# Kernel optimization log

Hardware: AMD Instinct MI355X
Metric: run time of the kernel (lower is better)

The kernel has to match this reference:

```python
import jax, jax.numpy as jnp
import numpy as np

N_EMBD = 512
N_HEAD = 8
EPS = 1e-5


def setup_inputs() -> dict:
    key = jax.random.key(0)
    ks = jax.random.split(key, 8)
    C = N_EMBD
    s = lambda k, shape, fan: jax.random.normal(k, shape, jnp.float32) * (1.0 / np.sqrt(fan))
    return {
        "x": jax.random.normal(ks[0], (2, 4096, C), jnp.float32),
        "w_qkv": s(ks[1], (C, 3 * C), C), "b_qkv": jnp.zeros((3 * C,), jnp.float32),
        "w_attn_proj": s(ks[2], (C, C), C), "b_attn_proj": jnp.zeros((C,), jnp.float32),
        "w_fc": s(ks[3], (C, 4 * C), C), "b_fc": jnp.zeros((4 * C,), jnp.float32),
        "w_mlp_proj": s(ks[4], (4 * C, C), 4 * C), "b_mlp_proj": jnp.zeros((C,), jnp.float32),
        "ln1_g": jnp.ones((C,), jnp.float32), "ln1_b": jnp.zeros((C,), jnp.float32),
        "ln2_g": jnp.ones((C,), jnp.float32), "ln2_b": jnp.zeros((C,), jnp.float32),
    }


def _layernorm(x, g, b):
    mu = jnp.mean(x, axis=-1, keepdims=True)
    var = jnp.mean(jnp.square(x - mu), axis=-1, keepdims=True)
    return (x - mu) * jax.lax.rsqrt(var + EPS) * g + b


def _attention(x, w_qkv, b_qkv, w_proj, b_proj):
    B, T, C = x.shape
    hd = C // N_HEAD
    qkv = x @ w_qkv + b_qkv  # [B,T,3C]
    q, k, v = jnp.split(qkv, 3, axis=-1)
    q = q.reshape(B, T, N_HEAD, hd)
    k = k.reshape(B, T, N_HEAD, hd)
    v = v.reshape(B, T, N_HEAD, hd)
    # NOTE: faithful to source -- scale by sqrt(C) (n_embd), not sqrt(head_dim)
    scores = jnp.einsum('bthd,bshd->bhts', q, k) / jnp.sqrt(jnp.float32(C))
    mask = jnp.tril(jnp.ones((T, T), bool))
    scores = jnp.where(mask, scores, -jnp.inf)
    attn = jax.nn.softmax(scores, axis=-1)  # [B,H,T,T]
    y = jnp.einsum('bhts,bshd->bthd', attn, v).reshape(B, T, C)
    return y @ w_proj + b_proj


def _mlp(x, w_fc, b_fc, w_proj, b_proj):
    h = jax.nn.gelu(x @ w_fc + b_fc, approximate=True)
    return h @ w_proj + b_proj


def reference(x, w_qkv, b_qkv, w_attn_proj, b_attn_proj, w_fc, b_fc,
              w_mlp_proj, b_mlp_proj, ln1_g, ln1_b, ln2_g, ln2_b):
    x = x + _attention(_layernorm(x, ln1_g, ln1_b), w_qkv, b_qkv, w_attn_proj, b_attn_proj)
    x = x + _mlp(_layernorm(x, ln2_g, ln2_b), w_fc, b_fc, w_mlp_proj, b_mlp_proj)
    return x
```

## Files before the change

kernel.cpp:

```cpp
#include <hip/hip_runtime.h>
#include <hip/hip_bf16.h>
#include <math.h>

constexpr int B_ = 2;
constexpr int T_ = 4096;
constexpr int C_ = 512;
constexpr int H_ = 8;
constexpr int BT_ = B_ * T_;
constexpr float EPS_ = 1e-5f;

typedef __attribute__((ext_vector_type(8))) short bf16x8;
typedef __attribute__((ext_vector_type(4))) short short4v;
typedef __attribute__((ext_vector_type(8))) short short8v;
typedef __attribute__((ext_vector_type(4))) float f32x4;

__device__ __forceinline__ short f2bf(float f) {
    unsigned int u = __float_as_uint(f);
    unsigned int r = (u + 0x7fffu + ((u >> 16) & 1u)) >> 16;
    return (short)r;
}
__device__ __forceinline__ float bf2f(short s) {
    return __uint_as_float(((unsigned)(unsigned short)s) << 16);
}
__device__ __forceinline__ short f2bf_h(float f) {
    union { __hip_bfloat16 h; short s; } u;
    u.h = __float2bfloat16(f);
    return u.s;
}
__device__ __forceinline__ float exp2_f(float x) {
    float r;
    asm("v_exp_f32 %0, %1" : "=v"(r) : "v"(x));
    return r;
}

__device__ __forceinline__ float gelu_f(float v) {
    const float k0 = 0.7978845608028654f;
    const float k1 = 0.044715f;
    return 0.5f * v * (1.0f + tanhf(k0 * (v + k1 * v * v * v)));
}

__device__ __forceinline__ void gl_lds16(const short* gsrc, short* lds) {
    __builtin_amdgcn_global_load_lds(
        (const __attribute__((address_space(1))) void*)gsrc,
        (__attribute__((address_space(3))) void*)lds, 16, 0, 0);
}

__global__ __launch_bounds__(256) void transpose_w4(
    const float* __restrict__ W0, short* __restrict__ D0,
    const float* __restrict__ W1, short* __restrict__ D1,
    const float* __restrict__ W2, short* __restrict__ D2,
    const float* __restrict__ W3, short* __restrict__ D3) {
    __shared__ float tile[32][33];
    int bid = blockIdx.x;
    const float* W; short* D; int K, N, nx;
    if (bid < 768)       {             W = W0; D = D0; K = 512;  N = 1536; nx = 48; }
    else if (bid < 1024) { bid -= 768;  W = W1; D = D1; K = 512;  N = 512;  nx = 16; }
    else if (bid < 2048) { bid -= 1024; W = W2; D = D2; K = 512;  N = 2048; nx = 64; }
    else                 { bid -= 2048; W = W3; D = D3; K = 2048; N = 512;  nx = 16; }
    const int n0 = (bid % nx) * 32, k0 = (bid / nx) * 32;
    const int tx = threadIdx.x & 31, ty = threadIdx.x >> 5;
    #pragma unroll
    for (int j = 0; j < 4; j++)
        tile[ty + j * 8][tx] = W[(size_t)(k0 + ty + j * 8) * N + n0 + tx];
    __syncthreads();
    #pragma unroll
    for (int j = 0; j < 4; j++)
        D[(size_t)(n0 + ty + j * 8) * K + k0 + tx] = f2bf(tile[tx][ty + j * 8]);
}

__global__ __launch_bounds__(256) void ln_bf16(const float* __restrict__ x,
                                               const float* __restrict__ g,
                                               const float* __restrict__ b,
                                               short* __restrict__ out) {
    const int row = blockIdx.x * 4 + (threadIdx.x >> 6);
    const int lane = threadIdx.x & 63;
    const float* xr = x + (size_t)row * C_;

    float4 v0 = *(const float4*)(xr + lane * 8);
    float4 v1 = *(const float4*)(xr + lane * 8 + 4);

    float s  = v0.x + v0.y + v0.z + v0.w + v1.x + v1.y + v1.z + v1.w;
    float s2 = v0.x*v0.x + v0.y*v0.y + v0.z*v0.z + v0.w*v0.w
             + v1.x*v1.x + v1.y*v1.y + v1.z*v1.z + v1.w*v1.w;
    #pragma unroll
    for (int off = 32; off; off >>= 1) {
        s  += __shfl_down(s, off);
        s2 += __shfl_down(s2, off);
    }
    s  = __shfl(s, 0);
    s2 = __shfl(s2, 0);

    const float mu  = s * (1.0f / C_);
    const float var = s2 * (1.0f / C_) - mu * mu;
    const float rs  = rsqrtf(var + EPS_);

    float4 g0 = *(const float4*)(g + lane * 8);
    float4 g1 = *(const float4*)(g + lane * 8 + 4);
    float4 b0 = *(const float4*)(b + lane * 8);
    float4 b1 = *(const float4*)(b + lane * 8 + 4);

    short8v o;
    o[0] = f2bf((v0.x - mu) * rs * g0.x + b0.x);
    o[1] = f2bf((v0.y - mu) * rs * g0.y + b0.y);
    o[2] = f2bf((v0.z - mu) * rs * g0.z + b0.z);
    o[3] = f2bf((v0.w - mu) * rs * g0.w + b0.w);
    o[4] = f2bf((v1.x - mu) * rs * g1.x + b1.x);
    o[5] = f2bf((v1.y - mu) * rs * g1.y + b1.y);
    o[6] = f2bf((v1.z - mu) * rs * g1.z + b1.z);
    o[7] = f2bf((v1.w - mu) * rs * g1.w + b1.w);
    *(short8v*)(out + (size_t)row * C_ + lane * 8) = o;
}

template<int BM, int ACT, int OUTBF16, int HASRES, int VFUSE>
__global__ __launch_bounds__(256) void gemm_bf16(const short* __restrict__ A,
                                                 const short* __restrict__ Wt,
                                                 const float* __restrict__ bias,
                                                 const float* __restrict__ res,
                                                 void* __restrict__ outp,
                                                 int M, int N, int K,
                                                 int GX, int CY,
                                                 short* __restrict__ vtb) {
    constexpr int BK   = (BM == 128) ? 64 : 128;
    constexpr int MT   = BM / 32;
    constexpr int JMAX = BK / 32;
    constexpr int CPR  = BK / 8;
    constexpr int RPI  = 256 / CPR;
    constexpr int AISS = BM / RPI;
    constexpr int BISS = 128 / RPI;

    __shared__ short As[BM * BK];
    __shared__ short Bs[128 * BK];

    const int bid = blockIdx.x;
    const int xcd = bid & 7, jb = bid >> 3;
    const int by = xcd * CY + jb / GX;
    const int bx = jb % GX;

    const int t = threadIdx.x;
    const int w = t >> 6;
    const int l = t & 63;
    const int c = l & 15;
    const int g = l >> 4;
    const int wr = w >> 1, wc = w & 1;
    const int m0 = by * BM, n0 = bx * 128;

    const int rt  = t / CPR;
    const int sch = ((t % CPR) ^ (rt & 7)) * 8;
    const short* Asrc = A  + (size_t)(m0 + rt) * K + sch;
    const short* Bsrc = Wt + (size_t)(n0 + rt) * K + sch;

    auto stage = [&](int kt) {
        #pragma unroll
        for (int i = 0; i < AISS; i++)
            gl_lds16(Asrc + (size_t)(RPI * i) * K + kt, &As[i * 2048 + w * 512]);
        #pragma unroll
        for (int i = 0; i < BISS; i++)
            gl_lds16(Bsrc + (size_t)(RPI * i) * K + kt, &Bs[i * 2048 + w * 512]);
    };

    f32x4 acc[MT][4] = {};

    for (int kt = 0; kt < K; kt += BK) {
        stage(kt);
        __syncthreads();

        #pragma unroll
        for (int j = 0; j < JMAX; j++) {
            const int ckj = ((4 * j + g) ^ (c & 7)) * 8;
            bf16x8 af[MT], bfr[4];
            #pragma unroll
            for (int mt = 0; mt < MT; mt++)
                af[mt] = *(const bf16x8*)&As[(wr * (BM / 2) + mt * 16 + c) * BK + ckj];
            #pragma unroll
            for (int nt = 0; nt < 4; nt++)
                bfr[nt] = *(const bf16x8*)&Bs[(wc * 64 + nt * 16 + c) * BK + ckj];
            #pragma unroll
            for (int mt = 0; mt < MT; mt++)
                #pragma unroll
                for (int nt = 0; nt < 4; nt++)
                    acc[mt][nt] = __builtin_amdgcn_mfma_f32_16x16x32_bf16(
                        af[mt], bfr[nt], acc[mt][nt], 0, 0, 0);
        }

        __syncthreads();
    }

    const int colb = n0 + wc * 64;
    float bias_v[4];
    #pragma unroll
    for (int nt = 0; nt < 4; nt++) bias_v[nt] = bias[colb + nt * 16 + c];

    if (VFUSE && n0 >= 1024) {
        const int bq   = m0 >> 12;
        const int trow = (m0 & 4095) + wr * (BM / 2);
        #pragma unroll
        for (int mt = 0; mt < MT; mt++) {
            const int tb = trow + (mt >> 1) * 32 + 8 * g + 4 * (mt & 1);
            #pragma unroll
            for (int nt = 0; nt < 4; nt++) {
                const int vcol = colb + nt * 16 + c - 1024;
                const int hh = vcol >> 6, dd = vcol & 63;
                short4v pk;
                #pragma unroll
                for (int rr = 0; rr < 4; rr++)
                    pk[rr] = f2bf(acc[mt][nt][rr] + bias_v[nt]);
                *(short4v*)&vtb[((size_t)((bq * 8 + hh) * 64 + dd)) * T_ + tb] = pk;
            }
        }
        return;
    }

    float* out_f = (float*)outp;
    short* out_h = (short*)outp;

    #pragma unroll
    for (int mt = 0; mt < MT; mt++) {
        #pragma unroll
        for (int rr = 0; rr < 4; rr++) {
            const size_t row = (size_t)(m0 + wr * (BM / 2) + mt * 16 + 4 * g + rr);
            #pragma unroll
            for (int nt = 0; nt < 4; nt++) {
                const int col = colb + nt * 16 + c;
                float v = acc[mt][nt][rr] + bias_v[nt];
                if (ACT) v = gelu_f(v);
                if (HASRES) v += res[row * N + col];
                if (OUTBF16) out_h[row * N + col] = f2bf(v);
                else         out_f[row * N + col] = v;
            }
        }
    }
}

__global__ __launch_bounds__(256) void attn_mfma(const short* __restrict__ qkv,
                                                 const short* __restrict__ Vt,
                                                 short* __restrict__ y) {
    __shared__ union {
        struct { short K[2][64 * 64]; short V[2][64 * 64]; } s;
        float O[4][16][68];
    } sm;

    const int bid = blockIdx.x;
    const int xcd = bid & 7, jj = bid >> 3;
    const int lo = jj >> 6;
    const int qtr = jj & 63;
    const int qt = (qtr < 32) ? (63 - qtr) : (qtr - 32);
    const int g16 = xcd * 2 + lo;
    const int b = g16 >> 3, h = g16 & 7;

    const int tid = threadIdx.x, w = tid >> 6, lid = tid & 63;
    const int c = lid & 15, g = lid >> 4;
    const size_t base = (size_t)b * T_;
    const int bh = g16;

    const float qmul = 0.04419417382415922f * 1.4426950408889634f;

    bf16x8 qf0, qf1;
    {
        const short* qa = qkv + (base + qt * 64 + w * 16 + c) * 1536 + h * 64 + g * 8;
        bf16x8 a0 = *(const bf16x8*)qa;
        bf16x8 a1 = *(const bf16x8*)(qa + 32);
        #pragma unroll
        for (int i = 0; i < 8; i++) {
            qf0[i] = f2bf_h(bf2f(a0[i]) * qmul);
            qf1[i] = f2bf_h(bf2f(a1[i]) * qmul);
        }
    }

    const f32x4 kZero = {0.f, 0.f, 0.f, 0.f};
    bf16x8 kOnes;
    #pragma unroll
    for (int i = 0; i < 8; i++) kOnes[i] = (short)0x3F80;

    f32x4 ot[4] = {};
    f32x4 lacc = {0.f, 0.f, 0.f, 0.f};
    const int qg = qt * 64 + w * 16 + c;

    const int sr = tid >> 3;
    const int sc = ((tid & 7) ^ (sr & 7)) * 8;

    auto stage = [&](short* Kb, short* Vb, int st) {
        const short* ks = qkv + (base + st * 64 + sr) * 1536 + 512 + h * 64 + sc;
        const short* vs = Vt + ((size_t)(bh * 64 + sr)) * T_ + st * 64 + sc;
        gl_lds16(ks, Kb + w * 512);
        gl_lds16(ks + (size_t)32 * 1536, Kb + 2048 + w * 512);
        gl_lds16(vs, Vb + w * 512);
        gl_lds16(vs + (size_t)32 * T_, Vb + 2048 + w * 512);
    };

    const int rx = c & 7;
    const int ck0 = g ^ rx;
    const int ck1 = ck0 ^ 4;

    auto tile = [&](const short* Kb, const short* Vb, bool mask_diag) {
        f32x4 s[4];
        __builtin_amdgcn_s_setprio(1);
        #pragma unroll
        for (int mt = 0; mt < 4; mt++) {
            const short* krow = Kb + (mt * 16 + c) * 64;
            bf16x8 k0 = *(const bf16x8*)&krow[ck0 * 8];
            bf16x8 k1 = *(const bf16x8*)&krow[ck1 * 8];
            f32x4 z = __builtin_amdgcn_mfma_f32_16x16x32_bf16(k0, qf0, kZero, 0, 0, 0);
            s[mt] = __builtin_amdgcn_mfma_f32_16x16x32_bf16(k1, qf1, z, 0, 0, 0);
        }
        __builtin_amdgcn_s_setprio(0);

        float p[4][4];
        #pragma unroll
        for (int mt = 0; mt < 4; mt++)
            #pragma unroll
            for (int rr = 0; rr < 4; rr++) {
                float v = s[mt][rr];
                if (mask_diag && (qt * 64 + mt * 16 + 4 * g + rr > qg)) v = -1e30f;
                p[mt][rr] = exp2_f(v);
            }

        bf16x8 pb0, pb1;
        #pragma unroll
        for (int i = 0; i < 8; i++) {
            pb0[i] = f2bf_h(p[(i >> 2)][i & 3]);
            pb1[i] = f2bf_h(p[2 + (i >> 2)][i & 3]);
        }
        __builtin_amdgcn_s_setprio(1);
        lacc = __builtin_amdgcn_mfma_f32_16x16x32_bf16(kOnes, pb0, lacc, 0, 0, 0);
        lacc = __builtin_amdgcn_mfma_f32_16x16x32_bf16(kOnes, pb1, lacc, 0, 0, 0);
        #pragma unroll
        for (int dt = 0; dt < 4; dt++) {
            const short* vrow = Vb + (16 * dt + c) * 64;
            bf16x8 va0 = *(const bf16x8*)&vrow[ck0 * 8];
            bf16x8 va1 = *(const bf16x8*)&vrow[ck1 * 8];
            ot[dt] = __builtin_amdgcn_mfma_f32_16x16x32_bf16(va0, pb0, ot[dt], 0, 0, 0);
            ot[dt] = __builtin_amdgcn_mfma_f32_16x16x32_bf16(va1, pb1, ot[dt], 0, 0, 0);
        }
        __builtin_amdgcn_s_setprio(0);
    };

    short* K0 = sm.s.K[0]; short* K1 = sm.s.K[1];
    short* V0 = sm.s.V[0]; short* V1 = sm.s.V[1];

    stage(K0, V0, 0);
    asm volatile("s_waitcnt vmcnt(0)" ::: "memory");
    __syncthreads();

    int st = 0;
    while (st + 2 <= qt) {
        stage(K1, V1, st + 1);
        tile(K0, V0, false);
        asm volatile("s_waitcnt vmcnt(0)" ::: "memory");
        __syncthreads();
        stage(K0, V0, st + 2);
        tile(K1, V1, false);
        asm volatile("s_waitcnt vmcnt(0)" ::: "memory");
        __syncthreads();
        st += 2;
    }
    if (st < qt) {
        stage(K1, V1, st + 1);
        tile(K0, V0, false);
        asm volatile("s_waitcnt vmcnt(0)" ::: "memory");
        __syncthreads();
        tile(K1, V1, true);
    } else {
        tile(K0, V0, true);
    }
    __syncthreads();

    const float inv = 1.0f / lacc[0];
    #pragma unroll
    for (int dt = 0; dt < 4; dt++)
        #pragma unroll
        for (int rr = 0; rr < 4; rr++)
            sm.O[w][c][16 * dt + 4 * g + rr] = ot[dt][rr] * inv;
    const int q = lid >> 2, ch = lid & 3;
    short* dst = y + (base + qt * 64 + w * 16 + q) * 512 + h * 64 + ch * 16;
    short8v o0, o1;
    #pragma unroll
    for (int j = 0; j < 8; j++) o0[j] = f2bf(sm.O[w][q][ch * 16 + j]);
    #pragma unroll
    for (int j = 0; j < 8; j++) o1[j] = f2bf(sm.O[w][q][ch * 16 + 8 + j]);
    *(short8v*)dst = o0;
    *(short8v*)(dst + 8) = o1;
}

extern "C" void kernel_launch(void* const* d_in, const int* in_sizes, int n_in,
                              void* d_out, int out_size, void* d_ws, size_t ws_size,
                              hipStream_t stream) {
    const float* x           = (const float*)d_in[0];
    const float* w_qkv       = (const float*)d_in[1];
    const float* b_qkv       = (const float*)d_in[2];
    const float* w_attn_proj = (const float*)d_in[3];
    const float* b_attn_proj = (const float*)d_in[4];
    const float* w_fc        = (const float*)d_in[5];
    const float* b_fc        = (const float*)d_in[6];
    const float* w_mlp_proj  = (const float*)d_in[7];
    const float* b_mlp_proj  = (const float*)d_in[8];
    const float* ln1_g       = (const float*)d_in[9];
    const float* ln1_b       = (const float*)d_in[10];
    const float* ln2_g       = (const float*)d_in[11];
    const float* ln2_b       = (const float*)d_in[12];

    float* out = (float*)d_out;
    short* ws16 = (short*)d_ws;

    short* wqkvT = ws16;
    short* waT   = wqkvT + 1536 * 512;
    short* wfcT  = waT   + 512 * 512;
    short* wmT   = wfcT  + 2048 * 512;
    short* xn    = wmT   + 512 * 2048;
    short* ybuf  = xn    + (size_t)BT_ * 512;
    short* qkvh  = ybuf  + (size_t)BT_ * 512;
    short* vtb   = qkvh  + (size_t)BT_ * 2048;

    transpose_w4<<<3072, 256, 0, stream>>>(w_qkv, wqkvT, w_attn_proj, waT,
                                           w_fc, wfcT, w_mlp_proj, wmT);

    ln_bf16<<<BT_ / 4, 256, 0, stream>>>(x, ln1_g, ln1_b, xn);

    gemm_bf16<128, 0, 1, 0, 1><<<12 * 64, 256, 0, stream>>>(
        xn, wqkvT, b_qkv, nullptr, qkvh, BT_, 1536, 512, 12, 8, vtb);

    attn_mfma<<<1024, 256, 0, stream>>>(qkvh, vtb, ybuf);

    gemm_bf16<64, 0, 0, 1, 0><<<4 * 128, 256, 0, stream>>>(
        ybuf, waT, b_attn_proj, x, out, BT_, 512, 512, 4, 16, nullptr);

    ln_bf16<<<BT_ / 4, 256, 0, stream>>>(out, ln2_g, ln2_b, xn);

    gemm_bf16<128, 1, 1, 0, 0><<<16 * 64, 256, 0, stream>>>(
        xn, wfcT, b_fc, nullptr, qkvh, BT_, 2048, 512, 16, 8, nullptr);

    gemm_bf16<64, 0, 0, 1, 0><<<4 * 128, 256, 0, stream>>>(
        qkvh, wmT, b_mlp_proj, out, out, BT_, 512, 2048, 4, 16, nullptr);
}
```

Measured before the change: 175.2 us.

## Split-K the MLP down-projection with atomics and shrink GEMM row tiles

Adds a SPLITK template option to the bf16 GEMM. Each block handles half of K and atomically adds its partial sums into the fp32 output, which already holds the residual, and only the first half adds the bias. The MLP down-projection (K=2048) now launches twice as many blocks, and the QKV and FC GEMMs move from 128-row to 64-row tiles for more blocks. The goal is better CU occupancy and load balance, at the cost of many global fp32 atomics, more redundant B-tile loads, and a nondeterministic summation order.

```diff
diff --git a/kernel.cpp b/kernel.cpp
--- a/kernel.cpp
+++ b/kernel.cpp
@@ -111,7 +111,7 @@
     *(short8v*)(out + (size_t)row * C_ + lane * 8) = o;
 }
 
-template<int BM, int ACT, int OUTBF16, int HASRES, int VFUSE>
+template<int BM, int ACT, int OUTBF16, int HASRES, int VFUSE, int SPLITK>
 __global__ __launch_bounds__(256) void gemm_bf16(const short* __restrict__ A,
                                                  const short* __restrict__ Wt,
                                                  const float* __restrict__ bias,
@@ -132,7 +132,10 @@
     __shared__ short Bs[128 * BK];
 
     const int bid = blockIdx.x;
-    const int xcd = bid & 7, jb = bid >> 3;
+    const int xcd = bid & 7;
+    int jb = bid >> 3;
+    int koff = 0;
+    if (SPLITK) { koff = (jb & 1) * (K >> 1); jb >>= 1; }
     const int by = xcd * CY + jb / GX;
     const int bx = jb % GX;
 
@@ -160,7 +163,8 @@
 
     f32x4 acc[MT][4] = {};
 
-    for (int kt = 0; kt < K; kt += BK) {
+    const int kend = SPLITK ? (koff + (K >> 1)) : K;
+    for (int kt = koff; kt < kend; kt += BK) {
         stage(kt);
         __syncthreads();
 
@@ -212,6 +216,24 @@
 
     float* out_f = (float*)outp;
     short* out_h = (short*)outp;
+
+    if (SPLITK) {
+        const bool addb = (koff == 0);
+        #pragma unroll
+        for (int mt = 0; mt < MT; mt++) {
+            #pragma unroll
+            for (int rr = 0; rr < 4; rr++) {
+                const size_t row = (size_t)(m0 + wr * (BM / 2) + mt * 16 + 4 * g + rr);
+                #pragma unroll
+                for (int nt = 0; nt < 4; nt++) {
+                    const int col = colb + nt * 16 + c;
+                    float v = acc[mt][nt][rr] + (addb ? bias_v[nt] : 0.0f);
+                    atomicAdd(&out_f[row * N + col], v);
+                }
+            }
+        }
+        return;
+    }
 
     #pragma unroll
     for (int mt = 0; mt < MT; mt++) {
@@ -415,19 +437,19 @@
 
     ln_bf16<<<BT_ / 4, 256, 0, stream>>>(x, ln1_g, ln1_b, xn);
 
-    gemm_bf16<128, 0, 1, 0, 1><<<12 * 64, 256, 0, stream>>>(
-        xn, wqkvT, b_qkv, nullptr, qkvh, BT_, 1536, 512, 12, 8, vtb);
+    gemm_bf16<64, 0, 1, 0, 1, 0><<<12 * 128, 256, 0, stream>>>(
+        xn, wqkvT, b_qkv, nullptr, qkvh, BT_, 1536, 512, 12, 16, vtb);
 
     attn_mfma<<<1024, 256, 0, stream>>>(qkvh, vtb, ybuf);
 
-    gemm_bf16<64, 0, 0, 1, 0><<<4 * 128, 256, 0, stream>>>(
+    gemm_bf16<64, 0, 0, 1, 0, 0><<<4 * 128, 256, 0, stream>>>(
         ybuf, waT, b_attn_proj, x, out, BT_, 512, 512, 4, 16, nullptr);
 
     ln_bf16<<<BT_ / 4, 256, 0, stream>>>(out, ln2_g, ln2_b, xn);
 
-    gemm_bf16<128, 1, 1, 0, 0><<<16 * 64, 256, 0, stream>>>(
-        xn, wfcT, b_fc, nullptr, qkvh, BT_, 2048, 512, 16, 8, nullptr);
-
-    gemm_bf16<64, 0, 0, 1, 0><<<4 * 128, 256, 0, stream>>>(
-        qkvh, wmT, b_mlp_proj, out, out, BT_, 512, 2048, 4, 16, nullptr);
-}
+    gemm_bf16<64, 1, 1, 0, 0, 0><<<16 * 128, 256, 0, stream>>>(
+        xn, wfcT, b_fc, nullptr, qkvh, BT_, 2048, 512, 16, 16, nullptr);
+
+    gemm_bf16<64, 0, 0, 0, 0, 1><<<1024, 256, 0, stream>>>(
+        qkvh, wmT, b_mlp_proj, nullptr, out, BT_, 512, 2048, 4, 16, nullptr);
+}
```

New measurement: 189.7 us. 1.08x slower.
